# Kernel tuning notes

Measured on AMD Instinct MI355X. Metric: run time of the kernel, lower is better.

The kernel has to match this reference:

```python
import jax, jax.numpy as jnp
import numpy as np

B, D, E, H, L, T = 512, 64, 512, 1024, 2, 96
LN_EPS = 1e-5


def setup_inputs() -> dict:
    key = jax.random.key(0)
    ks = jax.random.split(key, 20)
    r = lambda k, shape, sc=0.05: (jax.random.normal(k, shape, jnp.float32) * sc)
    inp = {
        "x_0": jax.random.normal(ks[0], (B, D), jnp.float32),
        "h_n": jax.random.normal(ks[1], (L, B, H), jnp.float32) * 0.1,
        "c_n": jax.random.normal(ks[2], (L, B, H), jnp.float32) * 0.1,
        "forecast_window": T,
        # share_embedding: Linear(D -> E)
        "emb_W": r(ks[3], (D, E)),
        "emb_b": r(ks[4], (E,)),
        # LSTM layer 0: input E -> hidden H ; gates order (i, f, g, o)
        "W_ih0": r(ks[5], (E, 4 * H)),
        "W_hh0": r(ks[6], (H, 4 * H)),
        "b_ih0": r(ks[7], (4 * H,)),
        "b_hh0": r(ks[8], (4 * H,)),
        # LSTM layer 1: input H -> hidden H
        "W_ih1": r(ks[9], (H, 4 * H)),
        "W_hh1": r(ks[10], (H, 4 * H)),
        "b_ih1": r(ks[11], (4 * H,)),
        "b_hh1": r(ks[12], (4 * H,)),
        # fc: Linear(H,H) -> LayerNorm(H) -> ReLU -> Linear(H,D)
        "fc1_W": r(ks[13], (H, H)),
        "fc1_b": r(ks[14], (H,)),
        "ln_g": jnp.ones((H,), jnp.float32),
        "ln_b": jnp.zeros((H,), jnp.float32),
        "fc2_W": r(ks[15], (H, D)),
        "fc2_b": r(ks[16], (D,)),
    }
    return inp


def _lstm_cell(x, h, c, Wih, Whh, b):
    gates = x @ Wih + h @ Whh + b  # [B, 4H]
    i, f, g, o = jnp.split(gates, 4, axis=-1)
    c2 = jax.nn.sigmoid(f) * c + jax.nn.sigmoid(i) * jnp.tanh(g)
    h2 = jax.nn.sigmoid(o) * jnp.tanh(c2)
    return h2, c2


def reference(x_0, h_n, c_n, forecast_window, emb_W, emb_b,
              W_ih0, W_hh0, b_ih0, b_hh0, W_ih1, W_hh1, b_ih1, b_hh1,
              fc1_W, fc1_b, ln_g, ln_b, fc2_W, fc2_b):
    b0 = b_ih0 + b_hh0
    b1 = b_ih1 + b_hh1

    def step(carry, _):
        x, h0, c0, h1, c1 = carry
        xe = x @ emb_W + emb_b                      # embedding
        h0, c0 = _lstm_cell(xe, h0, c0, W_ih0, W_hh0, b0)
        h1, c1 = _lstm_cell(h0, h1, c1, W_ih1, W_hh1, b1)
        z = h1 @ fc1_W + fc1_b                      # Linear
        mu = jnp.mean(z, axis=-1, keepdims=True)    # LayerNorm
        var = jnp.mean((z - mu) ** 2, axis=-1, keepdims=True)
        z = (z - mu) * jax.lax.rsqrt(var + LN_EPS) * ln_g + ln_b
        y = jax.nn.relu(z) @ fc2_W + fc2_b          # ReLU -> Linear
        return (y, h0, c0, h1, c1), y

    carry0 = (x_0, h_n[0], c_n[0], h_n[1], c_n[1])
    _, ys = jax.lax.scan(step, carry0, None, length=int(forecast_window))
    return jnp.transpose(ys, (1, 0, 2))  # [B, T, D]
```

## Files before the change

kernel.cpp:

```cpp
#include <hip/hip_runtime.h>
#include <hip/hip_bf16.h>

using bf16 = __hip_bfloat16;
using short8 = __attribute__((ext_vector_type(8))) short;
using f32x4 = __attribute__((ext_vector_type(4))) float;

#define BB 512
#define HH 1024
#define DD 64
#define TT 96

__device__ __forceinline__ void load_lds16(const void* g, void* l) {
  __builtin_amdgcn_global_load_lds(
      (const __attribute__((address_space(1))) unsigned int*)g,
      (__attribute__((address_space(3))) unsigned int*)l, 16, 0, 0);
}

__device__ __forceinline__ float sigm(float x) { return 1.0f / (1.0f + __expf(-x)); }
__device__ __forceinline__ float tanh_f(float x) {
  float e = __expf(2.0f * x);
  return 1.0f - 2.0f / (e + 1.0f);
}
__device__ __forceinline__ float wred(float v) {
#pragma unroll
  for (int m = 1; m < 64; m <<= 1) v += __shfl_xor(v, m, 64);
  return v;
}

__device__ __forceinline__ int gate_perm(int c) {
  int g = c >> 10, n = c & 1023;
  return (n >> 4) * 64 + g * 16 + (n & 15);
}


__global__ __launch_bounds__(256) void init_states_k(
    const float* __restrict__ x0, const float* __restrict__ hn, const float* __restrict__ cn,
    bf16* __restrict__ xbh, bf16* __restrict__ xbl,
    bf16* __restrict__ h0h, bf16* __restrict__ h0l,
    bf16* __restrict__ h1h, bf16* __restrict__ h1l,
    float* __restrict__ c0, float* __restrict__ c1)
{
  int i = blockIdx.x * 256 + threadIdx.x;
  if (i < BB * HH) {
    float v0 = hn[i];
    bf16 a0 = __float2bfloat16(v0);
    h0h[i] = a0; h0l[i] = __float2bfloat16(v0 - __bfloat162float(a0));
    float v1 = hn[BB * HH + i];
    bf16 a1 = __float2bfloat16(v1);
    h1h[i] = a1; h1l[i] = __float2bfloat16(v1 - __bfloat162float(a1));
    c0[i] = cn[i];
    c1[i] = cn[BB * HH + i];
  }
  if (i < BB * DD) {
    float v = x0[i];
    bf16 a = __float2bfloat16(v);
    xbh[i] = a; xbl[i] = __float2bfloat16(v - __bfloat162float(a));
  }
}

__global__ __launch_bounds__(256) void fold_emb_k(
    const float* __restrict__ embW, const float* __restrict__ embB,
    const float* __restrict__ Wih0, const float* __restrict__ bih0, const float* __restrict__ bhh0,
    bf16* __restrict__ W0h, bf16* __restrict__ W0l, float* __restrict__ bias0)
{
  __shared__ float sW[512 * 8];
  __shared__ float sb[512];
  int tid = threadIdx.x;
  int d0 = blockIdx.y * 8;
  for (int i = tid; i < 4096; i += 256) {
    int j = i >> 9;
    int e = i & 511;
    sW[e * 8 + j] = embW[(size_t)(d0 + j) * 512 + e];
  }
  for (int i = tid; i < 512; i += 256) sb[i] = embB[i];
  __syncthreads();
  int c = blockIdx.x * 256 + tid;
  float acc[8] = {0, 0, 0, 0, 0, 0, 0, 0};
  float bacc = 0.0f;
  for (int e = 0; e < 512; ++e) {
    float wv = Wih0[(size_t)e * 4096 + c];
    float4 wa = *(const float4*)&sW[e * 8];
    float4 wb = *(const float4*)&sW[e * 8 + 4];
    acc[0] += wa.x * wv; acc[1] += wa.y * wv; acc[2] += wa.z * wv; acc[3] += wa.w * wv;
    acc[4] += wb.x * wv; acc[5] += wb.y * wv; acc[6] += wb.z * wv; acc[7] += wb.w * wv;
    bacc += sb[e] * wv;
  }
  int pr = gate_perm(c);
#pragma unroll
  for (int j = 0; j < 8; ++j) {
    float v = acc[j];
    bf16 h = __float2bfloat16(v);
    W0h[(size_t)pr * 1088 + d0 + j] = h;
    W0l[(size_t)pr * 1088 + d0 + j] = __float2bfloat16(v - __bfloat162float(h));
  }
  if (blockIdx.y == 0) bias0[pr] = bacc + bih0[c] + bhh0[c];
}

template <bool PERM>
__global__ __launch_bounds__(256) void transpose_conv_k(
    const float* __restrict__ src, int N,
    bf16* __restrict__ dsth, bf16* __restrict__ dstl, int dstStride, int k0)
{
  __shared__ float tb[32][33];
  int tx = threadIdx.x & 31;
  int ty = threadIdx.x >> 5;
  int c0 = blockIdx.x * 32;
  int kk0 = blockIdx.y * 32;
#pragma unroll
  for (int q = 0; q < 4; ++q) {
    int k = kk0 + q * 8 + ty;
    tb[q * 8 + ty][tx] = src[(size_t)k * N + c0 + tx];
  }
  __syncthreads();
#pragma unroll
  for (int q = 0; q < 4; ++q) {
    int cc = c0 + q * 8 + ty;
    int pr = PERM ? gate_perm(cc) : cc;
    float v = tb[tx][q * 8 + ty];
    bf16 h = __float2bfloat16(v);
    size_t di = (size_t)pr * dstStride + k0 + kk0 + tx;
    dsth[di] = h;
    dstl[di] = __float2bfloat16(v - __bfloat162float(h));
  }
}

__global__ __launch_bounds__(256) void bias_perm_k(
    const float* __restrict__ a, const float* __restrict__ b, float* __restrict__ out)
{
  int c = blockIdx.x * 256 + threadIdx.x;
  out[gate_perm(c)] = a[c] + b[c];
}

template <int EPI>
__global__ __launch_bounds__(128) void gemm_pipe_k(
    const bf16* __restrict__ A1h, const bf16* __restrict__ A1l, int lda1, int K1len,
    const bf16* __restrict__ A2h, const bf16* __restrict__ A2l, int lda2,
    const bf16* __restrict__ Bh, const bf16* __restrict__ Bl, int KTOT,
    const float* __restrict__ bias,
    float* __restrict__ zout, float* __restrict__ cst,
    bf16* __restrict__ hho, bf16* __restrict__ hlo,
    int nPanels)
{
  __shared__ __align__(16) char smem[98304];
  const int tid = threadIdx.x, lane = tid & 63, wv = tid >> 6;
  const int bid = blockIdx.x;
  const int npanel = bid % nPanels;
  const int m0 = (bid / nPanels) * 64;
  const int nrow0 = npanel * 128;
  const int l15 = lane & 15, lhi = lane >> 4, kb = lhi * 16;

  f32x4 acc[16];
#pragma unroll
  for (int i = 0; i < 16; ++i) acc[i] = f32x4{0, 0, 0, 0};

  const int nt = KTOT >> 5;

  auto stage = [&](int buf, int kt) {
    char* lb = smem + buf * 24576;
    bool first = kt < K1len;
#pragma unroll
    for (int q = 0; q < 2; ++q) {
      int L = q * 128 + tid;
      int row = L >> 2, sl = L & 3;
      int sb = (sl * 16) ^ (((row >> 2) & 3) << 4);
      int ke = kt + (sb >> 1);
      const bf16* gh = first ? A1h + (size_t)(m0 + row) * lda1 + ke
                             : A2h + (size_t)(m0 + row) * lda2 + (ke - K1len);
      const bf16* gl = first ? A1l + (size_t)(m0 + row) * lda1 + ke
                             : A2l + (size_t)(m0 + row) * lda2 + (ke - K1len);
      load_lds16(gh, lb + L * 16);
      load_lds16(gl, lb + 4096 + L * 16);
    }
#pragma unroll
    for (int q = 0; q < 4; ++q) {
      int L = q * 128 + tid;
      int row = L >> 2, sl = L & 3;
      int sb = (sl * 16) ^ (((row >> 2) & 3) << 4);
      int ke = kt + (sb >> 1);
      load_lds16(Bh + (size_t)(nrow0 + row) * KTOT + ke, lb + 8192 + L * 16);
      load_lds16(Bl + (size_t)(nrow0 + row) * KTOT + ke, lb + 16384 + L * 16);
    }
  };

  stage(0, 0);
  if (nt > 1) stage(1, 32);
  if (nt > 2) stage(2, 64);

  for (int t = 0; t < nt; ++t) {
    int ahead = nt - 1 - t;
    if (ahead >= 2)      asm volatile("s_waitcnt vmcnt(24)" ::: "memory");
    else if (ahead == 1) asm volatile("s_waitcnt vmcnt(12)" ::: "memory");
    else                 asm volatile("s_waitcnt vmcnt(0)"  ::: "memory");
    asm volatile("s_waitcnt lgkmcnt(0)" ::: "memory");
    __builtin_amdgcn_s_barrier();
    __builtin_amdgcn_sched_barrier(0);
    if (t + 3 < nt) stage((t + 3) & 3, (t + 3) << 5);
    const char* base = smem + (t & 3) * 24576;
    short8 ah[4], al[4], bh[4], bl[4];
#pragma unroll
    for (int mf = 0; mf < 4; ++mf) {
      int arow = mf * 16 + l15;
      int aoff = arow * 64 + (kb ^ (((arow >> 2) & 3) << 4));
      ah[mf] = *(const short8*)(base + aoff);
      al[mf] = *(const short8*)(base + 4096 + aoff);
    }
#pragma unroll
    for (int nf = 0; nf < 4; ++nf) {
      int brow = wv * 64 + nf * 16 + l15;
      int boff = brow * 64 + (kb ^ (((brow >> 2) & 3) << 4));
      bh[nf] = *(const short8*)(base + 8192 + boff);
      bl[nf] = *(const short8*)(base + 16384 + boff);
    }
#pragma unroll
    for (int mf = 0; mf < 4; ++mf)
#pragma unroll
      for (int nf = 0; nf < 4; ++nf) {
        f32x4 c = acc[mf * 4 + nf];
        c = __builtin_amdgcn_mfma_f32_16x16x32_bf16(ah[mf], bh[nf], c, 0, 0, 0);
        c = __builtin_amdgcn_mfma_f32_16x16x32_bf16(ah[mf], bl[nf], c, 0, 0, 0);
        c = __builtin_amdgcn_mfma_f32_16x16x32_bf16(al[mf], bh[nf], c, 0, 0, 0);
        acc[mf * 4 + nf] = c;
      }
  }

  if (EPI == 0) {
    const int unit = npanel * 32 + wv * 16 + l15;
    const int prb = npanel * 128 + wv * 64 + l15;
    float bi = bias[prb + 0];
    float bfv = bias[prb + 16];
    float bg = bias[prb + 32];
    float bo = bias[prb + 48];
#pragma unroll
    for (int mf = 0; mf < 4; ++mf) {
      f32x4 ai = acc[mf * 4 + 0], af = acc[mf * 4 + 1];
      f32x4 ag = acc[mf * 4 + 2], ao = acc[mf * 4 + 3];
#pragma unroll
      for (int r = 0; r < 4; ++r) {
        int row = m0 + mf * 16 + lhi * 4 + r;
        size_t idx = (size_t)row * HH + unit;
        float iv = ai[r] + bi, fv = af[r] + bfv, gv = ag[r] + bg, ov = ao[r] + bo;
        float co = cst[idx];
        float cn2 = sigm(fv) * co + sigm(iv) * tanh_f(gv);
        cst[idx] = cn2;
        float hv = sigm(ov) * tanh_f(cn2);
        bf16 hh = __float2bfloat16(hv);
        hho[idx] = hh;
        hlo[idx] = __float2bfloat16(hv - __bfloat162float(hh));
      }
    }
  } else {
#pragma unroll
    for (int mf = 0; mf < 4; ++mf)
#pragma unroll
      for (int nf = 0; nf < 4; ++nf) {
        int col = npanel * 128 + wv * 64 + nf * 16 + l15;
        float bb = bias[col];
#pragma unroll
        for (int r = 0; r < 4; ++r) {
          int row = m0 + mf * 16 + lhi * 4 + r;
          zout[(size_t)row * HH + col] = acc[mf * 4 + nf][r] + bb;
        }
      }
  }
}

__global__ __launch_bounds__(256) void ln_fc2_k(
    const float* __restrict__ z, const float* __restrict__ lng, const float* __restrict__ lnb,
    const float* __restrict__ W2 , const float* __restrict__ b2,
    float* __restrict__ out ,
    bf16* __restrict__ xbh, bf16* __restrict__ xbl, int tstep)
{
  __shared__ float sa[4][1024];
  __shared__ float red[4][4][64];
  int tid = threadIdx.x, lane = tid & 63, w = tid >> 6;
  int row = blockIdx.x * 4 + w;
  float zv[16];
#pragma unroll
  for (int j = 0; j < 16; ++j) zv[j] = z[(size_t)row * 1024 + j * 64 + lane];
  float s = 0;
#pragma unroll
  for (int j = 0; j < 16; ++j) s += zv[j];
  s = wred(s);
  float mu = s * (1.0f / 1024.0f);
  float vs = 0;
#pragma unroll
  for (int j = 0; j < 16; ++j) { float d = zv[j] - mu; vs += d * d; }
  vs = wred(vs);
  float rstd = rsqrtf(vs * (1.0f / 1024.0f) + 1e-5f);
#pragma unroll
  for (int j = 0; j < 16; ++j) {
    int k = j * 64 + lane;
    float a = (zv[j] - mu) * rstd * lng[k] + lnb[k];
    sa[w][k] = a > 0.0f ? a : 0.0f;
  }
  __syncthreads();
  int n = tid & 63, ks = (tid >> 6) * 256;
  float p0 = 0, p1 = 0, p2 = 0, p3 = 0;
  for (int k = ks; k < ks + 256; ++k) {
    float wv2 = W2[(size_t)k * 64 + n];
    p0 += sa[0][k] * wv2; p1 += sa[1][k] * wv2; p2 += sa[2][k] * wv2; p3 += sa[3][k] * wv2;
  }
  int sl = tid >> 6;
  red[0][sl][n] = p0; red[1][sl][n] = p1; red[2][sl][n] = p2; red[3][sl][n] = p3;
  __syncthreads();
  int rr = tid >> 6;
  float y = red[rr][0][n] + red[rr][1][n] + red[rr][2][n] + red[rr][3][n] + b2[n];
  int orow = blockIdx.x * 4 + rr;
  out[((size_t)orow * TT + tstep) * DD + n] = y;
  bf16 hh = __float2bfloat16(y);
  xbh[(size_t)orow * DD + n] = hh;
  xbl[(size_t)orow * DD + n] = __float2bfloat16(y - __bfloat162float(hh));
}


extern "C" void kernel_launch(void* const* d_in, const int* in_sizes, int n_in,
                              void* d_out, int out_size, void* d_ws, size_t ws_size,
                              hipStream_t stream)
{
  const float* x0   = (const float*)d_in[0];
  const float* hn   = (const float*)d_in[1];
  const float* cn   = (const float*)d_in[2];
  const float* embW = (const float*)d_in[4];
  const float* embB = (const float*)d_in[5];
  const float* Wih0 = (const float*)d_in[6];
  const float* Whh0 = (const float*)d_in[7];
  const float* bih0 = (const float*)d_in[8];
  const float* bhh0 = (const float*)d_in[9];
  const float* Wih1 = (const float*)d_in[10];
  const float* Whh1 = (const float*)d_in[11];
  const float* bih1 = (const float*)d_in[12];
  const float* bhh1 = (const float*)d_in[13];
  const float* fc1W = (const float*)d_in[14];
  const float* fc1b = (const float*)d_in[15];
  const float* lng  = (const float*)d_in[16];
  const float* lnb  = (const float*)d_in[17];
  const float* fc2W = (const float*)d_in[18];
  const float* fc2b = (const float*)d_in[19];

  char* wp = (char*)d_ws;
  size_t off = 0;
  auto alloc = [&](size_t bytes) -> void* {
    void* p = wp + off;
    off += (bytes + 255) & ~(size_t)255;
    return p;
  };

  bf16* W0th  = (bf16*)alloc((size_t)4096 * 1088 * 2);
  bf16* W0tl  = (bf16*)alloc((size_t)4096 * 1088 * 2);
  bf16* W1th  = (bf16*)alloc((size_t)4096 * 2048 * 2);
  bf16* W1tl  = (bf16*)alloc((size_t)4096 * 2048 * 2);
  bf16* f1h   = (bf16*)alloc((size_t)1024 * 1024 * 2);
  bf16* f1l   = (bf16*)alloc((size_t)1024 * 1024 * 2);
  float* bias0 = (float*)alloc(4096 * 4);
  float* bias1 = (float*)alloc(4096 * 4);
  bf16* xbh   = (bf16*)alloc((size_t)BB * DD * 2);
  bf16* xbl   = (bf16*)alloc((size_t)BB * DD * 2);
  bf16* h0h_a = (bf16*)alloc((size_t)BB * HH * 2);
  bf16* h0h_b = (bf16*)alloc((size_t)BB * HH * 2);
  bf16* h0l_a = (bf16*)alloc((size_t)BB * HH * 2);
  bf16* h0l_b = (bf16*)alloc((size_t)BB * HH * 2);
  bf16* h1h_a = (bf16*)alloc((size_t)BB * HH * 2);
  bf16* h1h_b = (bf16*)alloc((size_t)BB * HH * 2);
  bf16* h1l_a = (bf16*)alloc((size_t)BB * HH * 2);
  bf16* h1l_b = (bf16*)alloc((size_t)BB * HH * 2);
  float* c0   = (float*)alloc((size_t)BB * HH * 4);
  float* c1   = (float*)alloc((size_t)BB * HH * 4);
  float* z    = (float*)alloc((size_t)BB * HH * 4);

  init_states_k<<<2048, 256, 0, stream>>>(x0, hn, cn, xbh, xbl, h0h_a, h0l_a,
                                          h1h_a, h1l_a, c0, c1);
  fold_emb_k<<<dim3(16, 8), 256, 0, stream>>>(embW, embB, Wih0, bih0, bhh0, W0th, W0tl, bias0);
  transpose_conv_k<true><<<dim3(128, 32), 256, 0, stream>>>(Whh0, 4096, W0th, W0tl, 1088, 64);
  transpose_conv_k<true><<<dim3(128, 32), 256, 0, stream>>>(Wih1, 4096, W1th, W1tl, 2048, 0);
  transpose_conv_k<true><<<dim3(128, 32), 256, 0, stream>>>(Whh1, 4096, W1th, W1tl, 2048, 1024);
  transpose_conv_k<false><<<dim3(32, 32), 256, 0, stream>>>(fc1W, 1024, f1h, f1l, 1024, 0);
  bias_perm_k<<<16, 256, 0, stream>>>(bih1, bhh1, bias1);

  bf16* h0h[2] = {h0h_a, h0h_b};
  bf16* h0l[2] = {h0l_a, h0l_b};
  bf16* h1h[2] = {h1h_a, h1h_b};
  bf16* h1l[2] = {h1l_a, h1l_b};
  float* outp = (float*)d_out;

  for (int t = 0; t < TT; ++t) {
    int p = t & 1;
    gemm_pipe_k<0><<<256, 128, 0, stream>>>(
        xbh, xbl, DD, DD, h0h[p], h0l[p], HH, W0th, W0tl, 1088, bias0,
        nullptr, c0, h0h[p ^ 1], h0l[p ^ 1], 32);
    gemm_pipe_k<0><<<256, 128, 0, stream>>>(
        h0h[p ^ 1], h0l[p ^ 1], HH, HH, h1h[p], h1l[p], HH, W1th, W1tl, 2048, bias1,
        nullptr, c1, h1h[p ^ 1], h1l[p ^ 1], 32);
    gemm_pipe_k<1><<<64, 128, 0, stream>>>(
        h1h[p ^ 1], h1l[p ^ 1], HH, 1024, h1h[p ^ 1], h1l[p ^ 1], HH, f1h, f1l, 1024,
        fc1b, z, nullptr, nullptr, nullptr, 8);
    ln_fc2_k<<<128, 256, 0, stream>>>(z, lng, lnb, fc2W, fc2b, outp, xbh, xbl, t);
  }
}
```

Measured before the change: 11.52 ms.

## Replace LDS-staged GEMM with direct global-to-register pipelined MFMA kernels

The shared-memory staged GEMM (64x128 tiles, 128 threads, 4-deep LDS ring with global_load_lds) is replaced by kernels that load A and B fragments straight from global memory into registers, using a 3-deep register ring. Each wave now computes a 16-row by 64-column tile, launched with 512 blocks of 256 threads and a block-index swizzle meant to improve L2 reuse of weight panels. fc1 gets its own kernel with 16x32 tiles per wave. The aim is to raise parallelism and drop LDS and barrier overhead for these small-batch recurrent GEMMs. The cost is that operands are no longer shared through LDS, so global/L2 traffic goes up.

```diff
diff --git a/kernel.cpp b/kernel.cpp
--- a/kernel.cpp
+++ b/kernel.cpp
@@ -9,12 +9,6 @@
 #define HH 1024
 #define DD 64
 #define TT 96
-
-__device__ __forceinline__ void load_lds16(const void* g, void* l) {
-  __builtin_amdgcn_global_load_lds(
-      (const __attribute__((address_space(1))) unsigned int*)g,
-      (__attribute__((address_space(3))) unsigned int*)l, 16, 0, 0);
-}
 
 __device__ __forceinline__ float sigm(float x) { return 1.0f / (1.0f + __expf(-x)); }
 __device__ __forceinline__ float tanh_f(float x) {
@@ -68,8 +62,7 @@
   int tid = threadIdx.x;
   int d0 = blockIdx.y * 8;
   for (int i = tid; i < 4096; i += 256) {
-    int j = i >> 9;
-    int e = i & 511;
+    int j = i >> 9, e = i & 511;
     sW[e * 8 + j] = embW[(size_t)(d0 + j) * 512 + e];
   }
   for (int i = tid; i < 512; i += 256) sb[i] = embB[i];
@@ -131,136 +124,174 @@
   out[gate_perm(c)] = a[c] + b[c];
 }
 
-template <int EPI>
-__global__ __launch_bounds__(128) void gemm_pipe_k(
+struct GF { short8 ah, al, bh[4], bl[4]; };
+
+__global__ __launch_bounds__(256, 2) void gates_k(
     const bf16* __restrict__ A1h, const bf16* __restrict__ A1l, int lda1, int K1len,
     const bf16* __restrict__ A2h, const bf16* __restrict__ A2l, int lda2,
-    const bf16* __restrict__ Bh, const bf16* __restrict__ Bl, int KTOT,
+    const bf16* __restrict__ Bh, const bf16* __restrict__ Bl, int KTOT, int nt,
     const float* __restrict__ bias,
-    float* __restrict__ zout, float* __restrict__ cst,
-    bf16* __restrict__ hho, bf16* __restrict__ hlo,
-    int nPanels)
-{
-  __shared__ __align__(16) char smem[98304];
-  const int tid = threadIdx.x, lane = tid & 63, wv = tid >> 6;
-  const int bid = blockIdx.x;
-  const int npanel = bid % nPanels;
-  const int m0 = (bid / nPanels) * 64;
-  const int nrow0 = npanel * 128;
-  const int l15 = lane & 15, lhi = lane >> 4, kb = lhi * 16;
-
-  f32x4 acc[16];
-#pragma unroll
-  for (int i = 0; i < 16; ++i) acc[i] = f32x4{0, 0, 0, 0};
-
-  const int nt = KTOT >> 5;
-
-  auto stage = [&](int buf, int kt) {
-    char* lb = smem + buf * 24576;
-    bool first = kt < K1len;
-#pragma unroll
-    for (int q = 0; q < 2; ++q) {
-      int L = q * 128 + tid;
-      int row = L >> 2, sl = L & 3;
-      int sb = (sl * 16) ^ (((row >> 2) & 3) << 4);
-      int ke = kt + (sb >> 1);
-      const bf16* gh = first ? A1h + (size_t)(m0 + row) * lda1 + ke
-                             : A2h + (size_t)(m0 + row) * lda2 + (ke - K1len);
-      const bf16* gl = first ? A1l + (size_t)(m0 + row) * lda1 + ke
-                             : A2l + (size_t)(m0 + row) * lda2 + (ke - K1len);
-      load_lds16(gh, lb + L * 16);
-      load_lds16(gl, lb + 4096 + L * 16);
-    }
-#pragma unroll
-    for (int q = 0; q < 4; ++q) {
-      int L = q * 128 + tid;
-      int row = L >> 2, sl = L & 3;
-      int sb = (sl * 16) ^ (((row >> 2) & 3) << 4);
-      int ke = kt + (sb >> 1);
-      load_lds16(Bh + (size_t)(nrow0 + row) * KTOT + ke, lb + 8192 + L * 16);
-      load_lds16(Bl + (size_t)(nrow0 + row) * KTOT + ke, lb + 16384 + L * 16);
+    float* __restrict__ cst, bf16* __restrict__ hho, bf16* __restrict__ hlo)
+{
+  const int tid = threadIdx.x, bid = blockIdx.x;
+  const int lane = tid & 63, wv = tid >> 6;
+  const int x = bid & 7, pq = (bid >> 3) & 3, mg = bid >> 5;
+  const int panel = x + 8 * pq;
+  const int m0 = mg * 32 + (wv & 1) * 16;
+  const int wn = wv >> 1;
+  const int l15 = lane & 15, lhi = lane >> 4;
+
+  const bf16* pBh[4];
+  const bf16* pBl[4];
+#pragma unroll
+  for (int nf = 0; nf < 4; ++nf) {
+    size_t ro = (size_t)(panel * 128 + wn * 64 + nf * 16 + l15) * KTOT + lhi * 8;
+    pBh[nf] = Bh + ro;
+    pBl[nf] = Bl + ro;
+  }
+
+  f32x4 acc[4];
+#pragma unroll
+  for (int i = 0; i < 4; ++i) acc[i] = f32x4{0, 0, 0, 0};
+
+  auto ldt = [&](int t, GF& f) {
+    int kt = t << 5;
+    const bf16 *sh, *sl; int ko, ld;
+    if (kt < K1len) { sh = A1h; sl = A1l; ko = kt; ld = lda1; }
+    else            { sh = A2h; sl = A2l; ko = kt - K1len; ld = lda2; }
+    size_t o = (size_t)(m0 + l15) * ld + ko + lhi * 8;
+    f.ah = *(const short8*)(sh + o);
+    f.al = *(const short8*)(sl + o);
+#pragma unroll
+    for (int nf = 0; nf < 4; ++nf) {
+      f.bh[nf] = *(const short8*)(pBh[nf] + kt);
+      f.bl[nf] = *(const short8*)(pBl[nf] + kt);
     }
   };
 
-  stage(0, 0);
-  if (nt > 1) stage(1, 32);
-  if (nt > 2) stage(2, 64);
-
-  for (int t = 0; t < nt; ++t) {
-    int ahead = nt - 1 - t;
-    if (ahead >= 2)      asm volatile("s_waitcnt vmcnt(24)" ::: "memory");
-    else if (ahead == 1) asm volatile("s_waitcnt vmcnt(12)" ::: "memory");
-    else                 asm volatile("s_waitcnt vmcnt(0)"  ::: "memory");
-    asm volatile("s_waitcnt lgkmcnt(0)" ::: "memory");
-    __builtin_amdgcn_s_barrier();
-    __builtin_amdgcn_sched_barrier(0);
-    if (t + 3 < nt) stage((t + 3) & 3, (t + 3) << 5);
-    const char* base = smem + (t & 3) * 24576;
-    short8 ah[4], al[4], bh[4], bl[4];
-#pragma unroll
-    for (int mf = 0; mf < 4; ++mf) {
-      int arow = mf * 16 + l15;
-      int aoff = arow * 64 + (kb ^ (((arow >> 2) & 3) << 4));
-      ah[mf] = *(const short8*)(base + aoff);
-      al[mf] = *(const short8*)(base + 4096 + aoff);
-    }
+  auto cmp = [&](GF& f) {
 #pragma unroll
     for (int nf = 0; nf < 4; ++nf) {
-      int brow = wv * 64 + nf * 16 + l15;
-      int boff = brow * 64 + (kb ^ (((brow >> 2) & 3) << 4));
-      bh[nf] = *(const short8*)(base + 8192 + boff);
-      bl[nf] = *(const short8*)(base + 16384 + boff);
-    }
-#pragma unroll
-    for (int mf = 0; mf < 4; ++mf)
-#pragma unroll
-      for (int nf = 0; nf < 4; ++nf) {
-        f32x4 c = acc[mf * 4 + nf];
-        c = __builtin_amdgcn_mfma_f32_16x16x32_bf16(ah[mf], bh[nf], c, 0, 0, 0);
-        c = __builtin_amdgcn_mfma_f32_16x16x32_bf16(ah[mf], bl[nf], c, 0, 0, 0);
-        c = __builtin_amdgcn_mfma_f32_16x16x32_bf16(al[mf], bh[nf], c, 0, 0, 0);
-        acc[mf * 4 + nf] = c;
-      }
-  }
-
-  if (EPI == 0) {
-    const int unit = npanel * 32 + wv * 16 + l15;
-    const int prb = npanel * 128 + wv * 64 + l15;
-    float bi = bias[prb + 0];
-    float bfv = bias[prb + 16];
-    float bg = bias[prb + 32];
-    float bo = bias[prb + 48];
-#pragma unroll
-    for (int mf = 0; mf < 4; ++mf) {
-      f32x4 ai = acc[mf * 4 + 0], af = acc[mf * 4 + 1];
-      f32x4 ag = acc[mf * 4 + 2], ao = acc[mf * 4 + 3];
-#pragma unroll
-      for (int r = 0; r < 4; ++r) {
-        int row = m0 + mf * 16 + lhi * 4 + r;
-        size_t idx = (size_t)row * HH + unit;
-        float iv = ai[r] + bi, fv = af[r] + bfv, gv = ag[r] + bg, ov = ao[r] + bo;
-        float co = cst[idx];
-        float cn2 = sigm(fv) * co + sigm(iv) * tanh_f(gv);
-        cst[idx] = cn2;
-        float hv = sigm(ov) * tanh_f(cn2);
-        bf16 hh = __float2bfloat16(hv);
-        hho[idx] = hh;
-        hlo[idx] = __float2bfloat16(hv - __bfloat162float(hh));
-      }
-    }
-  } else {
-#pragma unroll
-    for (int mf = 0; mf < 4; ++mf)
-#pragma unroll
-      for (int nf = 0; nf < 4; ++nf) {
-        int col = npanel * 128 + wv * 64 + nf * 16 + l15;
-        float bb = bias[col];
-#pragma unroll
-        for (int r = 0; r < 4; ++r) {
-          int row = m0 + mf * 16 + lhi * 4 + r;
-          zout[(size_t)row * HH + col] = acc[mf * 4 + nf][r] + bb;
-        }
-      }
+      f32x4 c = acc[nf];
+      c = __builtin_amdgcn_mfma_f32_16x16x32_bf16(f.ah, f.bh[nf], c, 0, 0, 0);
+      c = __builtin_amdgcn_mfma_f32_16x16x32_bf16(f.ah, f.bl[nf], c, 0, 0, 0);
+      c = __builtin_amdgcn_mfma_f32_16x16x32_bf16(f.al, f.bh[nf], c, 0, 0, 0);
+      acc[nf] = c;
+    }
+  };
+
+  GF fa, fb, fc;
+  ldt(0, fa); ldt(1, fb); ldt(2, fc);
+  for (int t = 0; t < nt; t += 3) {
+    cmp(fa);
+    if (t + 3 < nt) ldt(t + 3, fa);
+    if (t + 1 < nt) {
+      cmp(fb);
+      if (t + 4 < nt) ldt(t + 4, fb);
+    }
+    if (t + 2 < nt) {
+      cmp(fc);
+      if (t + 5 < nt) ldt(t + 5, fc);
+    }
+  }
+
+  const int unit = panel * 32 + wn * 16 + l15;
+  const int prb = panel * 128 + wn * 64 + l15;
+  float bi = bias[prb + 0];
+  float bfv = bias[prb + 16];
+  float bg = bias[prb + 32];
+  float bo = bias[prb + 48];
+  f32x4 ai = acc[0], af = acc[1], ag = acc[2], ao = acc[3];
+#pragma unroll
+  for (int r = 0; r < 4; ++r) {
+    int row = m0 + lhi * 4 + r;
+    size_t idx = (size_t)row * HH + unit;
+    float iv = ai[r] + bi, fv = af[r] + bfv, gv = ag[r] + bg, ov = ao[r] + bo;
+    float co = cst[idx];
+    float cn2 = sigm(fv) * co + sigm(iv) * tanh_f(gv);
+    cst[idx] = cn2;
+    float hv = sigm(ov) * tanh_f(cn2);
+    bf16 hh = __float2bfloat16(hv);
+    hho[idx] = hh;
+    hlo[idx] = __float2bfloat16(hv - __bfloat162float(hh));
+  }
+}
+
+__global__ __launch_bounds__(256, 2) void fc1_k(
+    const bf16* __restrict__ Ah, const bf16* __restrict__ Al,
+    const bf16* __restrict__ Bh, const bf16* __restrict__ Bl,
+    const float* __restrict__ bias, float* __restrict__ z)
+{
+  const int tid = threadIdx.x, bid = blockIdx.x;
+  const int lane = tid & 63, wv = tid >> 6;
+  const int x = bid & 7, mg = bid >> 3;
+  const int nchunk = x + 8 * wv;
+  const int m0 = mg * 16, n0 = nchunk * 32;
+  const int l15 = lane & 15, lhi = lane >> 4;
+  const int nt = 32;
+
+  const bf16* pBh[2];
+  const bf16* pBl[2];
+#pragma unroll
+  for (int nf = 0; nf < 2; ++nf) {
+    size_t ro = (size_t)(n0 + nf * 16 + l15) * HH + lhi * 8;
+    pBh[nf] = Bh + ro;
+    pBl[nf] = Bl + ro;
+  }
+
+  f32x4 acc[2];
+  acc[0] = f32x4{0, 0, 0, 0};
+  acc[1] = f32x4{0, 0, 0, 0};
+
+  struct FF { short8 ah, al, bh[2], bl[2]; };
+
+  auto ldt = [&](int t, FF& f) {
+    int kt = t << 5;
+    size_t o = (size_t)(m0 + l15) * HH + kt + lhi * 8;
+    f.ah = *(const short8*)(Ah + o);
+    f.al = *(const short8*)(Al + o);
+#pragma unroll
+    for (int nf = 0; nf < 2; ++nf) {
+      f.bh[nf] = *(const short8*)(pBh[nf] + kt);
+      f.bl[nf] = *(const short8*)(pBl[nf] + kt);
+    }
+  };
+
+  auto cmp = [&](FF& f) {
+#pragma unroll
+    for (int nf = 0; nf < 2; ++nf) {
+      f32x4 c = acc[nf];
+      c = __builtin_amdgcn_mfma_f32_16x16x32_bf16(f.ah, f.bh[nf], c, 0, 0, 0);
+      c = __builtin_amdgcn_mfma_f32_16x16x32_bf16(f.ah, f.bl[nf], c, 0, 0, 0);
+      c = __builtin_amdgcn_mfma_f32_16x16x32_bf16(f.al, f.bh[nf], c, 0, 0, 0);
+      acc[nf] = c;
+    }
+  };
+
+  FF fa, fb, fc;
+  ldt(0, fa); ldt(1, fb); ldt(2, fc);
+  for (int t = 0; t < nt; t += 3) {
+    cmp(fa);
+    if (t + 3 < nt) ldt(t + 3, fa);
+    if (t + 1 < nt) {
+      cmp(fb);
+      if (t + 4 < nt) ldt(t + 4, fb);
+    }
+    if (t + 2 < nt) {
+      cmp(fc);
+      if (t + 5 < nt) ldt(t + 5, fc);
+    }
+  }
+
+#pragma unroll
+  for (int nf = 0; nf < 2; ++nf) {
+    int col = n0 + nf * 16 + l15;
+    float bb = bias[col];
+#pragma unroll
+    for (int r = 0; r < 4; ++r) {
+      int row = m0 + lhi * 4 + r;
+      z[(size_t)row * HH + col] = acc[nf][r] + bb;
+    }
   }
 }
 
@@ -384,15 +415,13 @@
 
   for (int t = 0; t < TT; ++t) {
     int p = t & 1;
-    gemm_pipe_k<0><<<256, 128, 0, stream>>>(
-        xbh, xbl, DD, DD, h0h[p], h0l[p], HH, W0th, W0tl, 1088, bias0,
-        nullptr, c0, h0h[p ^ 1], h0l[p ^ 1], 32);
-    gemm_pipe_k<0><<<256, 128, 0, stream>>>(
-        h0h[p ^ 1], h0l[p ^ 1], HH, HH, h1h[p], h1l[p], HH, W1th, W1tl, 2048, bias1,
-        nullptr, c1, h1h[p ^ 1], h1l[p ^ 1], 32);
-    gemm_pipe_k<1><<<64, 128, 0, stream>>>(
-        h1h[p ^ 1], h1l[p ^ 1], HH, 1024, h1h[p ^ 1], h1l[p ^ 1], HH, f1h, f1l, 1024,
-        fc1b, z, nullptr, nullptr, nullptr, 8);
+    gates_k<<<512, 256, 0, stream>>>(
+        xbh, xbl, DD, DD, h0h[p], h0l[p], HH, W0th, W0tl, 1088, 34, bias0,
+        c0, h0h[p ^ 1], h0l[p ^ 1]);
+    gates_k<<<512, 256, 0, stream>>>(
+        h0h[p ^ 1], h0l[p ^ 1], HH, HH, h1h[p], h1l[p], HH, W1th, W1tl, 2048, 64, bias1,
+        c1, h1h[p ^ 1], h1l[p ^ 1]);
+    fc1_k<<<256, 256, 0, stream>>>(h1h[p ^ 1], h1l[p ^ 1], f1h, f1l, fc1b, z);
     ln_fc2_k<<<128, 256, 0, stream>>>(z, lng, lnb, fc2W, fc2b, outp, xbh, xbl, t);
   }
 }
```

After: 24.59 ms. 114% more time.
